# Kernel tuning notes

Measured on AMD Instinct MI355X. Metric: run time of the kernel, lower is better.

Reference implementation:

```python
import jax, jax.numpy as jnp
import numpy as np

HEADS = 16
D_MODEL = 1024
HEAD_DIM = D_MODEL // HEADS


def setup_inputs() -> dict:
    key = jax.random.key(0)
    ks = jax.random.split(key, 11)
    B, S = 4, 2048
    scale_in = 1.0 / np.sqrt(HEAD_DIM)
    scale_out = 1.0 / np.sqrt(D_MODEL)
    return {
        "values": jax.random.normal(ks[0], (B, S, D_MODEL), dtype=jnp.float32),
        "keys": jax.random.normal(ks[1], (B, S, D_MODEL), dtype=jnp.float32),
        "query": jax.random.normal(ks[2], (B, S, D_MODEL), dtype=jnp.float32),
        "wq": jax.random.normal(ks[3], (HEAD_DIM, HEAD_DIM), dtype=jnp.float32) * scale_in,
        "bq": jax.random.normal(ks[4], (HEAD_DIM,), dtype=jnp.float32) * 0.01,
        "wk": jax.random.normal(ks[5], (HEAD_DIM, HEAD_DIM), dtype=jnp.float32) * scale_in,
        "bk": jax.random.normal(ks[6], (HEAD_DIM,), dtype=jnp.float32) * 0.01,
        "wv": jax.random.normal(ks[7], (HEAD_DIM, HEAD_DIM), dtype=jnp.float32) * scale_in,
        "bv": jax.random.normal(ks[8], (HEAD_DIM,), dtype=jnp.float32) * 0.01,
        "wo": jax.random.normal(ks[9], (D_MODEL, D_MODEL), dtype=jnp.float32) * scale_out,
        "bo": jax.random.normal(ks[10], (D_MODEL,), dtype=jnp.float32) * 0.01,
    }


def reference(values, keys, query, wq, bq, wk, bk, wv, bv, wo, bo):
    B, Sq = query.shape[0], query.shape[1]
    Sk, Sv = keys.shape[1], values.shape[1]
    # reshape to (n, s, h, d); per-head linear shares one [d,d] weight across heads
    v = values.reshape(B, Sv, HEADS, HEAD_DIM) @ wv.T + bv
    k = keys.reshape(B, Sk, HEADS, HEAD_DIM) @ wk.T + bk
    q = query.reshape(B, Sq, HEADS, HEAD_DIM) @ wq.T + bq
    # scores scaled by sqrt(d_model) (as in original, NOT sqrt(head_dim))
    energy = jnp.einsum("nqhd,nkhd->nhqk", q, k)
    attn = jax.nn.softmax(energy / jnp.sqrt(jnp.float32(D_MODEL)), axis=-1)
    out = jnp.einsum("nhqk,nkhd->nqhd", attn, v).reshape(B, Sq, D_MODEL)
    return out @ wo.T + bo
```

## Files before the change

kernel.cpp:

```cpp
#include <hip/hip_runtime.h>

typedef unsigned short u16;
typedef short  bfrag  __attribute__((ext_vector_type(8), may_alias));
typedef unsigned long long ull_a __attribute__((may_alias));
typedef int    int_a  __attribute__((may_alias));
typedef int    i4_a   __attribute__((ext_vector_type(4), may_alias));
typedef float  f4_a   __attribute__((ext_vector_type(4), may_alias));
typedef unsigned u32x2 __attribute__((ext_vector_type(2)));
typedef __attribute__((ext_vector_type(4)))  float facc4;
typedef __attribute__((ext_vector_type(16))) float facc16;

#define SEQ   2048
#define NHEAD 16
#define HD    64
#define DM    1024
#define BH    64
#define NTOK  8192
#define QSC   0.04508422f

#if defined(__has_builtin)
#if __has_builtin(__builtin_amdgcn_cvt_pk_bf16_f32)
#define HAS_CVT_PK 1
#endif
#if __has_builtin(__builtin_amdgcn_permlane32_swap)
#define HAS_PLSWAP 1
#endif
#endif
#ifndef HAS_CVT_PK
#define HAS_CVT_PK 0
#endif
#ifndef HAS_PLSWAP
#define HAS_PLSWAP 0
#endif

__device__ __forceinline__ u16 f2bf(float f){
  union { float f; unsigned u; } x; x.f = f;
  unsigned r = x.u + 0x7FFFu + ((x.u >> 16) & 1u);
  return (u16)(r >> 16);
}
__device__ __forceinline__ unsigned pk2(float a, float b){
#if HAS_CVT_PK
  auto r = __builtin_amdgcn_cvt_pk_bf16_f32(a, b);
  union { decltype(r) v; unsigned u; } x; x.v = r; return x.u;
#else
  return (unsigned)f2bf(a) | ((unsigned)f2bf(b) << 16);
#endif
}
__device__ __forceinline__ unsigned long long pk4(float a, float b, float c, float d){
  return (unsigned long long)pk2(a,b) | ((unsigned long long)pk2(c,d) << 32);
}
__device__ __forceinline__ void swap32(unsigned &a, unsigned &b){
#if HAS_PLSWAP
  u32x2 r = __builtin_amdgcn_permlane32_swap(a, b, false, false);
  a = r[0]; b = r[1];
#else
  int lane = threadIdx.x & 63; int hh = lane >> 5;
  unsigned pa = (unsigned)__shfl_xor((int)a, 32, 64);
  unsigned pb = (unsigned)__shfl_xor((int)b, 32, 64);
  unsigned na = hh ? pb : a;
  unsigned nb = hh ? b  : pa;
  a = na; b = nb;
#endif
}
__device__ __forceinline__ bfrag ld8f(const float* p){
  f4_a a = *(const f4_a*)p;
  f4_a b = *(const f4_a*)(p + 4);
  union { bfrag v; unsigned u[4]; } r;
  r.u[0] = pk2(a[0],a[1]); r.u[1] = pk2(a[2],a[3]);
  r.u[2] = pk2(b[0],b[1]); r.u[3] = pk2(b[2],b[3]);
  return r.v;
}
__device__ __forceinline__ void stage16(const u16* g, u16* l){
  __builtin_amdgcn_global_load_lds((const __attribute__((address_space(1))) void*)g,
                                   (__attribute__((address_space(3))) void*)l, 16, 0, 0);
}

__global__ __launch_bounds__(256) void k_wconv(
  const float* __restrict__ wo, const float* __restrict__ wq,
  const float* __restrict__ wk, const float* __restrict__ wv,
  u16* __restrict__ dst)
{
  long i = ((long)blockIdx.x * 256 + threadIdx.x) * 8;
  const float* src; long off;
  if      (i < 1048576)        { src = wo; off = i; }
  else if (i < 1048576+4096)   { src = wq; off = i - 1048576; }
  else if (i < 1048576+8192)   { src = wk; off = i - (1048576+4096); }
  else                         { src = wv; off = i - (1048576+8192); }
  f4_a a = *(const f4_a*)(src + off);
  f4_a b = *(const f4_a*)(src + off + 4);
  ull_a* p = (ull_a*)(dst + i);
  p[0] = pk4(a[0],a[1],a[2],a[3]);
  p[1] = pk4(b[0],b[1],b[2],b[3]);
}

__global__ __launch_bounds__(256) void k_proj(
  const float* __restrict__ vin, const float* __restrict__ kin, const float* __restrict__ qin,
  const u16* __restrict__ wqb, const u16* __restrict__ wkb, const u16* __restrict__ wvb,
  const float* __restrict__ bq, const float* __restrict__ bk, const float* __restrict__ bv,
  u16* __restrict__ qo, u16* __restrict__ ko, u16* __restrict__ vo)
{
  __shared__ __align__(16) u16 Lq[16*264], Lk[16*264], Lv[16*264];
  int tid  = threadIdx.x;
  int wid  = tid >> 6, lane = tid & 63;
  int quad = lane >> 4, col = lane & 15;
  int token = blockIdx.x * 4 + wid;
  int b  = (blockIdx.x * 4) >> 11;
  int s0 = (blockIdx.x * 4) & 2047;
  long xbase = (long)token * DM;

  bfrag aq[2], ak[2], av[2];
  #pragma unroll
  for (int ks = 0; ks < 2; ks++){
    long off = xbase + (long)col * HD + ks*32 + quad*8;
    aq[ks] = ld8f(qin + off);
    ak[ks] = ld8f(kin + off);
    av[ks] = ld8f(vin + off);
  }
  #pragma unroll
  for (int ns = 0; ns < 4; ns++){
    facc4 accq = {0.f,0.f,0.f,0.f}, acck = {0.f,0.f,0.f,0.f}, accv = {0.f,0.f,0.f,0.f};
    #pragma unroll
    for (int ks = 0; ks < 2; ks++){
      int woff = (ns*16 + col) * HD + ks*32 + quad*8;
      bfrag bwq = *(const bfrag*)(wqb + woff);
      bfrag bwk = *(const bfrag*)(wkb + woff);
      bfrag bwv = *(const bfrag*)(wvb + woff);
      accq = __builtin_amdgcn_mfma_f32_16x16x32_bf16(aq[ks], bwq, accq, 0,0,0);
      acck = __builtin_amdgcn_mfma_f32_16x16x32_bf16(ak[ks], bwk, acck, 0,0,0);
      accv = __builtin_amdgcn_mfma_f32_16x16x32_bf16(av[ks], bwv, accv, 0,0,0);
    }
    int d = ns*16 + col;
    float fbq = bq[d], fbk = bk[d], fbv = bv[d];
    #pragma unroll
    for (int r = 0; r < 4; r++){
      int h = quad*4 + r;
      int li = h*264 + wid*64 + d;
      Lq[li] = f2bf((accq[r] + fbq) * QSC);
      Lk[li] = f2bf(acck[r] + fbk);
      Lv[li] = f2bf(accv[r] + fbv);
    }
  }
  __syncthreads();
  int h = tid >> 4, c = tid & 15;
  int src = h*264 + c*16;
  long gb = ((long)(b*NHEAD + h) * SEQ + s0) * HD + c*16;
  *(i4_a*)(qo + gb)     = *(const i4_a*)&Lq[src];
  *(i4_a*)(qo + gb + 8) = *(const i4_a*)&Lq[src + 8];
  *(i4_a*)(ko + gb)     = *(const i4_a*)&Lk[src];
  *(i4_a*)(ko + gb + 8) = *(const i4_a*)&Lk[src + 8];
  *(i4_a*)(vo + gb)     = *(const i4_a*)&Lv[src];
  *(i4_a*)(vo + gb + 8) = *(const i4_a*)&Lv[src + 8];
}

__global__ __launch_bounds__(256) void k_vtrans(
  const u16* __restrict__ vin, u16* __restrict__ vt)
{
  __shared__ __align__(16) u16 T[64*264];
  int tid = threadIdx.x;
  int wid = tid >> 6, lane = tid & 63;
  int s0  = blockIdx.x * 256;
  int bh  = blockIdx.y;
  const u16* ip = vin + ((long)bh * SEQ + s0 + tid) * HD;
  #pragma unroll
  for (int j = 0; j < 8; j++){
    bfrag v8 = *(const bfrag*)(ip + j*8);
    #pragma unroll
    for (int i = 0; i < 8; i++)
      T[(j*8 + i)*264 + tid] = (u16)((short*)&v8)[i];
  }
  __syncthreads();
  long obase = (long)bh * HD * SEQ + s0;
  #pragma unroll
  for (int it = 0; it < 16; it++){
    int d = it*4 + wid;
    ull_a v = *(const ull_a*)&T[d*264 + lane*4];
    *(ull_a*)(vt + obase + (long)d * SEQ + lane*4) = v;
  }
}

__global__ __launch_bounds__(256, 4) void k_attn(
  const u16* __restrict__ qws, const u16* __restrict__ kws, const u16* __restrict__ vt,
  u16* __restrict__ aout)
{
  __shared__ __align__(16) u16 KV[2][2][64*64];
  int tid = threadIdx.x;
  int wid = tid >> 6, lane = tid & 63;
  int ln = lane & 31, hh = lane >> 5;
  int bh = blockIdx.y;
  int q0 = blockIdx.x * 128 + wid * 32;
  long base = (long)bh * SEQ * HD;

  int srow   = lane >> 3;
  int schunk = (lane & 7) ^ srow;

  bfrag qf[4];
  #pragma unroll
  for (int ks = 0; ks < 4; ks++)
    qf[ks] = *(const bfrag*)(qws + base + (long)(q0 + ln)*HD + ks*16 + hh*8);

  facc16 OO0, OO1;
  #pragma unroll
  for (int r = 0; r < 16; r++){ OO0[r] = 0.f; OO1[r] = 0.f; }
  float l_ = 0.f;

  #pragma unroll
  for (int g2 = 0; g2 < 2; g2++){
    int g = wid + g2*4;
    stage16(kws + base + (long)(g*8 + srow)*HD + schunk*8,       &KV[0][0][g*512]);
    stage16(vt  + base + (long)(g*8 + srow)*SEQ + schunk*8,      &KV[0][1][g*512]);
  }

  for (int kt = 0; kt < 32; kt++){
    int buf = kt & 1;
    __syncthreads();
    if (kt + 1 < 32){
      int k0n = (kt + 1) * 64;
      #pragma unroll
      for (int g2 = 0; g2 < 2; g2++){
        int g = wid + g2*4;
        stage16(kws + base + (long)(k0n + g*8 + srow)*HD + schunk*8, &KV[buf^1][0][g*512]);
        stage16(vt  + base + (long)(g*8 + srow)*SEQ + k0n + schunk*8, &KV[buf^1][1][g*512]);
      }
    }

    facc16 E0, E1;
    #pragma unroll
    for (int r = 0; r < 16; r++){ E0[r] = 0.f; E1[r] = 0.f; }
    __builtin_amdgcn_s_setprio(1);
    #pragma unroll
    for (int ks = 0; ks < 4; ks++){
      int sw = ((2*ks + hh) ^ (ln & 7)) * 8;
      bfrag kf0 = *(const bfrag*)&KV[buf][0][ ln      *64 + sw];
      bfrag kf1 = *(const bfrag*)&KV[buf][0][(32 + ln)*64 + sw];
      E0 = __builtin_amdgcn_mfma_f32_32x32x16_bf16(kf0, qf[ks], E0, 0,0,0);
      E1 = __builtin_amdgcn_mfma_f32_32x32x16_bf16(kf1, qf[ks], E1, 0,0,0);
    }
    __builtin_amdgcn_s_setprio(0);

    float rs = 0.f;
    #pragma unroll
    for (int r = 0; r < 16; r++){
      float p0 = __builtin_amdgcn_exp2f(E0[r]);
      float p1 = __builtin_amdgcn_exp2f(E1[r]);
      E0[r] = p0; E1[r] = p1; rs += p0 + p1;
    }
    l_ += rs;

    bfrag pf[4];
    #pragma unroll
    for (int half = 0; half < 2; half++){
      const facc16& P = half ? E1 : E0;
      #pragma unroll
      for (int k2 = 0; k2 < 2; k2++){
        int rb = k2 * 8;
        unsigned A0 = pk2(P[rb+0], P[rb+1]);
        unsigned A1 = pk2(P[rb+2], P[rb+3]);
        unsigned B0 = pk2(P[rb+4], P[rb+5]);
        unsigned B1 = pk2(P[rb+6], P[rb+7]);
        swap32(A0, B0);
        swap32(A1, B1);
        union { bfrag v; unsigned u[4]; } t;
        t.u[0] = A0; t.u[1] = A1; t.u[2] = B0; t.u[3] = B1;
        pf[half*2 + k2] = t.v;
      }
    }

    __builtin_amdgcn_s_setprio(1);
    #pragma unroll
    for (int ks = 0; ks < 4; ks++){
      int sw = ((2*ks + hh) ^ (ln & 7)) * 8;
      bfrag vf0 = *(const bfrag*)&KV[buf][1][ ln      *64 + sw];
      bfrag vf1 = *(const bfrag*)&KV[buf][1][(32 + ln)*64 + sw];
      OO0 = __builtin_amdgcn_mfma_f32_32x32x16_bf16(vf0, pf[ks], OO0, 0,0,0);
      OO1 = __builtin_amdgcn_mfma_f32_32x32x16_bf16(vf1, pf[ks], OO1, 0,0,0);
    }
    __builtin_amdgcn_s_setprio(0);
  }

  l_ += __shfl_xor(l_, 32, 64);
  float inv = 1.0f / l_;
  int b_ = bh >> 4, h_ = bh & 15;
  long orow = ((long)(b_ * SEQ + q0 + ln) * NHEAD + h_) * HD;
  #pragma unroll
  for (int g = 0; g < 4; g++){
    *(ull_a*)(aout + orow +      8*g + 4*hh) =
      pk4(OO0[4*g]*inv, OO0[4*g+1]*inv, OO0[4*g+2]*inv, OO0[4*g+3]*inv);
    *(ull_a*)(aout + orow + 32 + 8*g + 4*hh) =
      pk4(OO1[4*g]*inv, OO1[4*g+1]*inv, OO1[4*g+2]*inv, OO1[4*g+3]*inv);
  }
}

__global__ __launch_bounds__(256) void k_oproj(
  const u16* __restrict__ A, const u16* __restrict__ Bw,
  const float* __restrict__ bo, float* __restrict__ out)
{
  __shared__ __align__(16) u16 As[128*64];
  __shared__ __align__(16) u16 Bs[128*64];
  int tid  = threadIdx.x;
  int wid  = tid >> 6, lane = tid & 63;
  int quad = lane >> 4, col = lane & 15;
  int m0 = blockIdx.x * 128;
  int n0 = blockIdx.y * 128;
  int wm = (wid & 1) * 64, wn = (wid >> 1) * 64;

  facc4 acc[4][4];
  #pragma unroll
  for (int i = 0; i < 4; i++)
    #pragma unroll
    for (int j = 0; j < 4; j++) acc[i][j] = {0.f,0.f,0.f,0.f};

  int srow = wid*8 + (lane >> 3);
  int scol = (lane & 7) * 8;
  const u16* Ag = A  + (long)(m0 + srow) * DM + scol;
  const u16* Bg = Bw + (long)(n0 + srow) * DM + scol;

  for (int k0 = 0; k0 < DM; k0 += 64){
    __syncthreads();
    #pragma unroll
    for (int j = 0; j < 4; j++){
      stage16(Ag + (long)j*32*DM + k0, &As[(j*32 + wid*8)*64]);
      stage16(Bg + (long)j*32*DM + k0, &Bs[(j*32 + wid*8)*64]);
    }
    __syncthreads();

    #pragma unroll
    for (int ks = 0; ks < 2; ks++){
      bfrag af[4], bf[4];
      #pragma unroll
      for (int i = 0; i < 4; i++)
        af[i] = *(const bfrag*)&As[(wm + i*16 + col)*64 + ks*32 + quad*8];
      #pragma unroll
      for (int i = 0; i < 4; i++)
        bf[i] = *(const bfrag*)&Bs[(wn + i*16 + col)*64 + ks*32 + quad*8];
      #pragma unroll
      for (int i = 0; i < 4; i++)
        #pragma unroll
        for (int j = 0; j < 4; j++)
          acc[i][j] = __builtin_amdgcn_mfma_f32_16x16x32_bf16(af[i], bf[j], acc[i][j], 0,0,0);
    }
  }

  #pragma unroll
  for (int j = 0; j < 4; j++){
    int n = n0 + wn + j*16 + col;
    float bias = bo[n];
    #pragma unroll
    for (int i = 0; i < 4; i++){
      long mrow = m0 + wm + i*16 + quad*4;
      #pragma unroll
      for (int r = 0; r < 4; r++)
        out[(mrow + r) * DM + n] = acc[i][j][r] + bias;
    }
  }
}

extern "C" void kernel_launch(void* const* d_in, const int* in_sizes, int n_in,
                              void* d_out, int out_size, void* d_ws, size_t ws_size,
                              hipStream_t stream)
{
  const float* values = (const float*)d_in[0];
  const float* keys   = (const float*)d_in[1];
  const float* query  = (const float*)d_in[2];
  const float* wq = (const float*)d_in[3];
  const float* bq = (const float*)d_in[4];
  const float* wk = (const float*)d_in[5];
  const float* bk = (const float*)d_in[6];
  const float* wv = (const float*)d_in[7];
  const float* bv = (const float*)d_in[8];
  const float* wo = (const float*)d_in[9];
  const float* bo = (const float*)d_in[10];

  const long N = 8388608;
  u16* qws  = (u16*)d_ws;
  u16* kws  = qws  + N;
  u16* vws  = kws  + N;
  u16* vtws = vws  + N;
  u16* wob  = vtws + N;
  u16* wqb  = wob + 1048576;
  u16* wkb  = wqb + 4096;
  u16* wvb  = wkb + 4096;
  u16* aws  = vws;

  k_wconv <<<518,           256, 0, stream>>>(wo, wq, wk, wv, wob);
  k_proj  <<<2048,          256, 0, stream>>>(values, keys, query, wqb, wkb, wvb,
                                              bq, bk, bv, qws, kws, vws);
  k_vtrans<<<dim3(8, 64),   256, 0, stream>>>(vws, vtws);
  k_attn  <<<dim3(16, 64),  256, 0, stream>>>(qws, kws, vtws, aws);
  k_oproj <<<dim3(64, 8),   256, 0, stream>>>(aws, wob, bo, (float*)d_out);
}
```

Measured before the change: 308.5 us.

## Use 512-thread attention blocks with XCD-aware block mapping

Attention blocks grow from 4 to 8 waves, so each block covers 256 queries and every K/V tile staged into shared memory is reused by twice as many waves. Each wave now stages one 8-row group per tile instead of two. The 1D grid is remapped so blocks sharing a (batch, head) land on the same XCD, aiming for better L2 reuse of K/V. The tile loop is manually unrolled by two so buffer indices are compile-time constants. The trade-off is fewer blocks (512 instead of 1024), higher per-CU register pressure, and a barrier that now synchronises more waves.

```diff
diff --git a/kernel.cpp b/kernel.cpp
--- a/kernel.cpp
+++ b/kernel.cpp
@@ -178,7 +178,7 @@
   }
 }
 
-__global__ __launch_bounds__(256, 4) void k_attn(
+__global__ __launch_bounds__(512, 4) void k_attn(
   const u16* __restrict__ qws, const u16* __restrict__ kws, const u16* __restrict__ vt,
   u16* __restrict__ aout)
 {
@@ -186,8 +186,10 @@
   int tid = threadIdx.x;
   int wid = tid >> 6, lane = tid & 63;
   int ln = lane & 31, hh = lane >> 5;
-  int bh = blockIdx.y;
-  int q0 = blockIdx.x * 128 + wid * 32;
+  int bid = blockIdx.x;
+  int xcd = bid & 7, lix = bid >> 3;
+  int bh = xcd * 8 + (lix >> 3);
+  int q0 = (lix & 7) * 256 + wid * 32;
   long base = (long)bh * SEQ * HD;
 
   int srow   = lane >> 3;
@@ -203,24 +205,15 @@
   for (int r = 0; r < 16; r++){ OO0[r] = 0.f; OO1[r] = 0.f; }
   float l_ = 0.f;
 
-  #pragma unroll
-  for (int g2 = 0; g2 < 2; g2++){
-    int g = wid + g2*4;
-    stage16(kws + base + (long)(g*8 + srow)*HD + schunk*8,       &KV[0][0][g*512]);
-    stage16(vt  + base + (long)(g*8 + srow)*SEQ + schunk*8,      &KV[0][1][g*512]);
-  }
-
-  for (int kt = 0; kt < 32; kt++){
-    int buf = kt & 1;
+  stage16(kws + base + (long)(wid*8 + srow)*HD + schunk*8,  &KV[0][0][wid*512]);
+  stage16(vt  + base + (long)(wid*8 + srow)*SEQ + schunk*8, &KV[0][1][wid*512]);
+
+  auto tile = [&](int buf, int kt){
     __syncthreads();
     if (kt + 1 < 32){
       int k0n = (kt + 1) * 64;
-      #pragma unroll
-      for (int g2 = 0; g2 < 2; g2++){
-        int g = wid + g2*4;
-        stage16(kws + base + (long)(k0n + g*8 + srow)*HD + schunk*8, &KV[buf^1][0][g*512]);
-        stage16(vt  + base + (long)(g*8 + srow)*SEQ + k0n + schunk*8, &KV[buf^1][1][g*512]);
-      }
+      stage16(kws + base + (long)(k0n + wid*8 + srow)*HD + schunk*8, &KV[buf^1][0][wid*512]);
+      stage16(vt  + base + (long)(wid*8 + srow)*SEQ + k0n + schunk*8, &KV[buf^1][1][wid*512]);
     }
 
     facc16 E0, E1;
@@ -275,6 +268,11 @@
       OO1 = __builtin_amdgcn_mfma_f32_32x32x16_bf16(vf1, pf[ks], OO1, 0,0,0);
     }
     __builtin_amdgcn_s_setprio(0);
+  };
+
+  for (int kt = 0; kt < 32; kt += 2){
+    tile(0, kt);
+    tile(1, kt + 1);
   }
 
   l_ += __shfl_xor(l_, 32, 64);
@@ -385,6 +383,6 @@
   k_proj  <<<2048,          256, 0, stream>>>(values, keys, query, wqb, wkb, wvb,
                                               bq, bk, bv, qws, kws, vws);
   k_vtrans<<<dim3(8, 64),   256, 0, stream>>>(vws, vtws);
-  k_attn  <<<dim3(16, 64),  256, 0, stream>>>(qws, kws, vtws, aws);
+  k_attn  <<<512,           512, 0, stream>>>(qws, kws, vtws, aws);
   k_oproj <<<dim3(64, 8),   256, 0, stream>>>(aws, wob, bo, (float*)d_out);
 }
```

New measurement: 307.0 us. No clear change (-0.5%).
